# Kernel tuning notes

Measured on AMD Instinct MI355X. Metric: run time of the kernel, lower is better.

Reference implementation:

```python
import jax, jax.numpy as jnp
import numpy as np

N_NODES = 500000
N_FEAT = 128
N_GRAPHS = 2048

def setup_inputs() -> dict:
    key = jax.random.key(0)
    k1, k2 = jax.random.split(key)
    x = jax.random.normal(k1, (N_NODES, N_FEAT), dtype=jnp.float32)
    batch = jnp.sort(jax.random.randint(k2, (N_NODES,), 0, N_GRAPHS, dtype=jnp.int64))
    p = jnp.ones((1,), dtype=jnp.float32)
    beta = jnp.ones((1,), dtype=jnp.float32)
    return {"x": x, "batch": batch, "p": p, "beta": beta, "bsize": N_GRAPHS}

def reference(x, batch, p, beta, bsize):
    # n_nodes per graph, broadcast to [B, F] (matches scatter_sum of ones_like(x))
    n_nodes = jax.ops.segment_sum(jnp.ones_like(x), batch, num_segments=bsize)
    # scatter_softmax over p * x.detach() within each graph segment
    logits = p * jax.lax.stop_gradient(x)                      # [N, F]
    seg_max = jax.ops.segment_max(logits, batch, num_segments=bsize)  # [B, F]
    e = jnp.exp(logits - seg_max[batch])                       # [N, F]
    denom = jax.ops.segment_sum(e, batch, num_segments=bsize)  # [B, F]
    w = e / denom[batch]                                       # [N, F]
    # weighted sum per graph, then generalized mean-max rescale
    out = jax.ops.segment_sum(x * w, batch, num_segments=bsize)  # [B, F]
    return out * n_nodes / (1.0 + beta * (n_nodes - 1.0))
```

## Files before the change

kernel.cpp:

```cpp
#include <hip/hip_runtime.h>
#include <math.h>

#define NFEAT 128
#define NGRAPHS 2048

__global__ void find_starts_kernel(const int* __restrict__ batch, int n,
                                   int* __restrict__ starts) {
    int i = blockIdx.x * blockDim.x + threadIdx.x;
    if (i >= n) return;
    int b = batch[i];
    int prev = (i == 0) ? -1 : batch[i - 1];
    for (int g = prev + 1; g <= b; ++g) starts[g] = i;
    if (i == n - 1) {
        for (int g = b + 1; g <= NGRAPHS; ++g) starts[g] = n;
    }
}

__global__ __launch_bounds__(256) void pool_kernel(
    const float* __restrict__ x, const int* __restrict__ starts,
    const float* __restrict__ p_ptr, const float* __restrict__ beta_ptr,
    float* __restrict__ out) {
    const int g = blockIdx.x;
    const int s = starts[g];
    const int e = starts[g + 1];
    const int cnt = e - s;
    const float p = p_ptr[0];
    const float beta = beta_ptr[0];

    const int lane = threadIdx.x & 31;
    const int rg = threadIdx.x >> 5;

    float m[4], d[4], num[4];
#pragma unroll
    for (int j = 0; j < 4; ++j) {
        m[j] = -INFINITY;
        d[j] = 0.0f;
        num[j] = 0.0f;
    }

    const float* __restrict__ xg = x + (size_t)s * NFEAT;
    for (int r = rg; r < cnt; r += 8) {
        const float4 v = *(const float4*)(xg + (size_t)r * NFEAT + lane * 4);
        float vals[4] = {v.x, v.y, v.z, v.w};
#pragma unroll
        for (int j = 0; j < 4; ++j) {
            float l = p * vals[j];
            float mn = fmaxf(m[j], l);
            float sc = __expf(m[j] - mn);
            float t = __expf(l - mn);
            d[j] = d[j] * sc + t;
            num[j] = num[j] * sc + vals[j] * t;
            m[j] = mn;
        }
    }

    __shared__ float sm[8][NFEAT];
    __shared__ float sd[8][NFEAT];
    __shared__ float sn[8][NFEAT];
#pragma unroll
    for (int j = 0; j < 4; ++j) {
        sm[rg][lane * 4 + j] = m[j];
        sd[rg][lane * 4 + j] = d[j];
        sn[rg][lane * 4 + j] = num[j];
    }
    __syncthreads();

    if (threadIdx.x < NFEAT) {
        const int f = threadIdx.x;
        float M = sm[0][f], D = sd[0][f], Nm = sn[0][f];
#pragma unroll
        for (int k = 1; k < 8; ++k) {
            float m2 = sm[k][f];
            float Mn = fmaxf(M, m2);
            float s1 = __expf(M - Mn);
            float s2 = __expf(m2 - Mn);
            D = D * s1 + sd[k][f] * s2;
            Nm = Nm * s1 + sn[k][f] * s2;
            M = Mn;
        }
        float n = (float)cnt;
        float rescale = n / (1.0f + beta * (n - 1.0f));
        out[(size_t)g * NFEAT + f] = (Nm / D) * rescale;
    }
}

extern "C" void kernel_launch(void* const* d_in, const int* in_sizes, int n_in,
                              void* d_out, int out_size, void* d_ws, size_t ws_size,
                              hipStream_t stream) {
    const float* x = (const float*)d_in[0];
    const int* batch = (const int*)d_in[1];
    const float* p = (const float*)d_in[2];
    const float* beta = (const float*)d_in[3];
    float* out = (float*)d_out;
    int* starts = (int*)d_ws;

    const int n = in_sizes[0] / NFEAT;

    find_starts_kernel<<<(n + 255) / 256, 256, 0, stream>>>(batch, n, starts);
    pool_kernel<<<NGRAPHS, 256, 0, stream>>>(x, starts, p, beta, out);
}
```

Before: 357.2 us.

## Fuse segment-start search into pool kernel and unroll row loads by four

Drops the separate find_starts kernel. Each block now binary-searches the sorted batch array for its own segment bounds, which removes one launch and its trip through global memory. The row loop is unrolled to issue four independent float4 loads before the online-softmax updates, which raises memory-level parallelism. In exchange, each block pays for two serial binary searches of about 19 dependent global loads before any streaming starts.

```diff
diff --git a/kernel.cpp b/kernel.cpp
--- a/kernel.cpp
+++ b/kernel.cpp
@@ -4,25 +4,40 @@
 #define NFEAT 128
 #define NGRAPHS 2048
 
-__global__ void find_starts_kernel(const int* __restrict__ batch, int n,
-                                   int* __restrict__ starts) {
-    int i = blockIdx.x * blockDim.x + threadIdx.x;
-    if (i >= n) return;
-    int b = batch[i];
-    int prev = (i == 0) ? -1 : batch[i - 1];
-    for (int g = prev + 1; g <= b; ++g) starts[g] = i;
-    if (i == n - 1) {
-        for (int g = b + 1; g <= NGRAPHS; ++g) starts[g] = n;
+__device__ __forceinline__ void update4(const float4& v, float p,
+                                        float* m, float* d, float* num) {
+    float vals[4] = {v.x, v.y, v.z, v.w};
+#pragma unroll
+    for (int j = 0; j < 4; ++j) {
+        float l = p * vals[j];
+        float mn = fmaxf(m[j], l);
+        float sc = __expf(m[j] - mn);
+        float t = __expf(l - mn);
+        d[j] = d[j] * sc + t;
+        num[j] = num[j] * sc + vals[j] * t;
+        m[j] = mn;
     }
 }
 
 __global__ __launch_bounds__(256) void pool_kernel(
-    const float* __restrict__ x, const int* __restrict__ starts,
+    const float* __restrict__ x, const int* __restrict__ batch, int n,
     const float* __restrict__ p_ptr, const float* __restrict__ beta_ptr,
     float* __restrict__ out) {
     const int g = blockIdx.x;
-    const int s = starts[g];
-    const int e = starts[g + 1];
+
+    __shared__ int sbounds[2];
+    if (threadIdx.x < 2) {
+        const int target = g + (int)threadIdx.x;
+        int lo = 0, hi = n;
+        while (lo < hi) {
+            int mid = (lo + hi) >> 1;
+            if (batch[mid] < target) lo = mid + 1; else hi = mid;
+        }
+        sbounds[threadIdx.x] = lo;
+    }
+    __syncthreads();
+    const int s = sbounds[0];
+    const int e = sbounds[1];
     const int cnt = e - s;
     const float p = p_ptr[0];
     const float beta = beta_ptr[0];
@@ -38,20 +53,22 @@
         num[j] = 0.0f;
     }
 
-    const float* __restrict__ xg = x + (size_t)s * NFEAT;
-    for (int r = rg; r < cnt; r += 8) {
-        const float4 v = *(const float4*)(xg + (size_t)r * NFEAT + lane * 4);
-        float vals[4] = {v.x, v.y, v.z, v.w};
-#pragma unroll
-        for (int j = 0; j < 4; ++j) {
-            float l = p * vals[j];
-            float mn = fmaxf(m[j], l);
-            float sc = __expf(m[j] - mn);
-            float t = __expf(l - mn);
-            d[j] = d[j] * sc + t;
-            num[j] = num[j] * sc + vals[j] * t;
-            m[j] = mn;
-        }
+    const float* __restrict__ bp = x + (size_t)s * NFEAT + lane * 4;
+
+    int r = rg;
+    for (; r + 24 < cnt; r += 32) {
+        const float4 c0 = *(const float4*)(bp + (size_t)(r     ) * NFEAT);
+        const float4 c1 = *(const float4*)(bp + (size_t)(r +  8) * NFEAT);
+        const float4 c2 = *(const float4*)(bp + (size_t)(r + 16) * NFEAT);
+        const float4 c3 = *(const float4*)(bp + (size_t)(r + 24) * NFEAT);
+        update4(c0, p, m, d, num);
+        update4(c1, p, m, d, num);
+        update4(c2, p, m, d, num);
+        update4(c3, p, m, d, num);
+    }
+    for (; r < cnt; r += 8) {
+        const float4 c0 = *(const float4*)(bp + (size_t)r * NFEAT);
+        update4(c0, p, m, d, num);
     }
 
     __shared__ float sm[8][NFEAT];
@@ -78,8 +95,8 @@
             Nm = Nm * s1 + sn[k][f] * s2;
             M = Mn;
         }
-        float n = (float)cnt;
-        float rescale = n / (1.0f + beta * (n - 1.0f));
+        float nn = (float)cnt;
+        float rescale = nn / (1.0f + beta * (nn - 1.0f));
         out[(size_t)g * NFEAT + f] = (Nm / D) * rescale;
     }
 }
@@ -92,10 +109,9 @@
     const float* p = (const float*)d_in[2];
     const float* beta = (const float*)d_in[3];
     float* out = (float*)d_out;
-    int* starts = (int*)d_ws;
+    (void)d_ws; (void)ws_size;
 
     const int n = in_sizes[0] / NFEAT;
 
-    find_starts_kernel<<<(n + 255) / 256, 256, 0, stream>>>(batch, n, starts);
-    pool_kernel<<<NGRAPHS, 256, 0, stream>>>(x, starts, p, beta, out);
+    pool_kernel<<<NGRAPHS, 256, 0, stream>>>(x, batch, n, p, beta, out);
 }
```

Result: no change. 359.3 us (+0.6%).
